# Performance work log

Measured on AMD Instinct MI355X. Metric: run time of the kernel, lower is better.

## Reference

```python
import jax, jax.numpy as jnp
import numpy as np

N = 32768          # total nodes
B = 64             # graphs
NPG = N // B       # nodes per graph (equal-sized graphs)
E = 524288         # edges (before self-loops)
D_IN, HID, HEADS, D_OUT = 128, 64, 4, 128
DH = HID * HEADS   # 256
NEG_SLOPE = 0.2
EPS = 1e-5

def _leaky(x):
    return jnp.where(x >= 0, x, NEG_SLOPE * x)

def gat_conv(x, src, dst, W, a_src, a_dst, b, concat):
    """PyG-style GATConv (self-loops already included in src/dst)."""
    H, C = a_src.shape
    h = (x @ W).reshape(N, H, C)                       # [N,H,C]
    es = jnp.einsum('nhc,hc->nh', h, a_src)            # score from source feats
    ed = jnp.einsum('nhc,hc->nh', h, a_dst)            # score from target feats
    e = _leaky(es[src] + ed[dst])                      # [E',H]
    m = jax.ops.segment_max(e, dst, num_segments=N)    # stable softmax per dst
    p = jnp.exp(e - m[dst])
    s = jax.ops.segment_sum(p, dst, num_segments=N)
    alpha = p / s[dst]                                 # [E',H]
    out = jax.ops.segment_sum(h[src] * alpha[..., None], dst, num_segments=N)
    out = out.reshape(N, H * C) if concat else out.mean(axis=1)
    return out + b

def mha(x, Wi, bi, Wo, bo, heads):
    """torch.nn.MultiheadAttention (batch_first, no mask, eval)."""
    Bb, T, D = x.shape
    qkv = x @ Wi.T + bi                                # [B,T,3D]
    q, k, v = jnp.split(qkv, 3, axis=-1)
    hd = D // heads
    def sp(t):
        return t.reshape(Bb, T, heads, hd).transpose(0, 2, 1, 3)  # [B,h,T,hd]
    q, k, v = sp(q), sp(k), sp(v)
    scores = jnp.einsum('bhqd,bhkd->bhqk', q, k) / jnp.sqrt(jnp.float32(hd))
    attn = jax.nn.softmax(scores, axis=-1)
    o = jnp.einsum('bhqk,bhkd->bhqd', attn, v)
    o = o.transpose(0, 2, 1, 3).reshape(Bb, T, D)
    return o @ Wo.T + bo

def layer_norm(x, g, b):
    mu = x.mean(-1, keepdims=True)
    var = x.var(-1, keepdims=True)
    return (x - mu) / jnp.sqrt(var + EPS) * g + b

def setup_inputs() -> dict:
    key = jax.random.key(0)
    ks = jax.random.split(key, 20)
    s = 0.1
    inp = {
        'x': jax.random.normal(ks[0], (N, D_IN), jnp.float32),
        'edge_index': jax.random.randint(ks[1], (2, E), 0, N, jnp.int64),
        'batch': (jnp.arange(N, dtype=jnp.int64) // NPG),
        # gat1: D_IN -> HEADS*HID (concat)
        'W1': jax.random.normal(ks[2], (D_IN, HEADS * HID), jnp.float32) * s,
        'aS1': jax.random.normal(ks[3], (HEADS, HID), jnp.float32) * s,
        'aD1': jax.random.normal(ks[4], (HEADS, HID), jnp.float32) * s,
        'b1': jnp.zeros((HEADS * HID,), jnp.float32),
        # gat2: DH -> HEADS*HID (concat)
        'W2': jax.random.normal(ks[5], (DH, HEADS * HID), jnp.float32) * s,
        'aS2': jax.random.normal(ks[6], (HEADS, HID), jnp.float32) * s,
        'aD2': jax.random.normal(ks[7], (HEADS, HID), jnp.float32) * s,
        'b2': jnp.zeros((HEADS * HID,), jnp.float32),
        # gat3: DH -> D_OUT, heads=1, concat=False (mean)
        'W3': jax.random.normal(ks[8], (DH, D_OUT), jnp.float32) * s,
        'aS3': jax.random.normal(ks[9], (1, D_OUT), jnp.float32) * s,
        'aD3': jax.random.normal(ks[10], (1, D_OUT), jnp.float32) * s,
        'b3': jnp.zeros((D_OUT,), jnp.float32),
        # MultiheadAttention
        'Wi': jax.random.normal(ks[11], (3 * DH, DH), jnp.float32) * s,
        'bi': jnp.zeros((3 * DH,), jnp.float32),
        'Wo': jax.random.normal(ks[12], (DH, DH), jnp.float32) * s,
        'bo': jnp.zeros((DH,), jnp.float32),
        # LayerNorm
        'gamma': jnp.ones((DH,), jnp.float32),
        'beta': jnp.zeros((DH,), jnp.float32),
    }
    return inp

def reference(x, edge_index, batch, W1, aS1, aD1, b1, W2, aS2, aD2, b2,
              W3, aS3, aD3, b3, Wi, bi, Wo, bo, gamma, beta):
    # add self-loops (PyG GATConv default)
    loops = jnp.arange(N, dtype=edge_index.dtype)
    src = jnp.concatenate([edge_index[0], loops])
    dst = jnp.concatenate([edge_index[1], loops])

    x1 = jax.nn.elu(gat_conv(x, src, dst, W1, aS1, aD1, b1, concat=True))
    x2 = jax.nn.elu(gat_conv(x1, src, dst, W2, aS2, aD2, b2, concat=True))

    # ragged-to-dense batching: batch = arange(N)//NPG (equal-sized, sorted),
    # so the torch python loop reduces to a reshape with no padding.
    x2b = x2.reshape(B, NPG, DH)
    attended = mha(x2b, Wi, bi, Wo, bo, HEADS).reshape(N, DH)

    x2a = layer_norm(attended + x2, gamma, beta)
    x3 = gat_conv(x2a, src, dst, W3, aS3, aD3, b3, concat=False)
    return x3
```

## Files before the change

kernel.cpp:

```cpp
#include <hip/hip_runtime.h>

typedef _Float16 half_t;
typedef _Float16 half8  __attribute__((ext_vector_type(8)));
typedef _Float16 half4v __attribute__((ext_vector_type(4)));
typedef _Float16 half2v __attribute__((ext_vector_type(2)));
typedef float    f32x4  __attribute__((ext_vector_type(4)));
typedef float    f32x2  __attribute__((ext_vector_type(2)));

constexpr int N_NODES = 32768;
constexpr int NPG_    = 512;

#define MFMA16(a, b, c) __builtin_amdgcn_mfma_f32_16x16x32_f16((a), (b), (c), 0, 0, 0)

#if defined(__has_builtin)
#  if __has_builtin(__builtin_amdgcn_cvt_pk_f16_fp8)
#    define HAVE_PK_F16_FP8 1
#  else
#    define HAVE_PK_F16_FP8 0
#  endif
#else
#  define HAVE_PK_F16_FP8 0
#endif

__device__ __forceinline__ void gload_lds16(const half_t* g, half_t* l) {
  __builtin_amdgcn_global_load_lds(
      (const __attribute__((address_space(1))) void*)g,
      (__attribute__((address_space(3))) void*)l, 16, 0, 0);
}

__device__ __forceinline__ void fp8x4_fma(int wrd, half2v p, half2v* acc) {
#if HAVE_PK_F16_FP8
  half2v lo = __builtin_amdgcn_cvt_pk_f16_fp8((short)(wrd & 0xffff));
  half2v hi = __builtin_amdgcn_cvt_pk_f16_fp8((short)(((unsigned)wrd) >> 16));
#else
  f32x2 flo = __builtin_amdgcn_cvt_pk_f32_fp8(wrd, false);
  f32x2 fhi = __builtin_amdgcn_cvt_pk_f32_fp8(wrd, true);
  half2v lo = {(half_t)flo.x, (half_t)flo.y};
  half2v hi = {(half_t)fhi.x, (half_t)fhi.y};
#endif
  acc[0] += p * lo;
  acc[1] += p * hi;
}

__global__ __launch_bounds__(256) void k_scan1(const int* __restrict__ deg,
                                               int* __restrict__ partial,
                                               int* __restrict__ blockSums) {
  __shared__ int sd[256];
  int t = threadIdx.x;
  int i = blockIdx.x * 256 + t;
  int v = deg[i] + 1;
  sd[t] = v;
  __syncthreads();
  int acc = v;
  for (int off = 1; off < 256; off <<= 1) {
    int add = (t >= off) ? sd[t - off] : 0;
    __syncthreads();
    acc += add;
    sd[t] = acc;
    __syncthreads();
  }
  partial[i] = acc - v;
  if (t == 255) blockSums[blockIdx.x] = acc;
}

__global__ __launch_bounds__(128) void k_scan2(const int* __restrict__ blockSums,
                                               int* __restrict__ blockOff,
                                               int* __restrict__ rowptr) {
  __shared__ int sd[128];
  int t = threadIdx.x;
  int v = blockSums[t];
  sd[t] = v;
  __syncthreads();
  for (int off = 1; off < 128; off <<= 1) {
    int add = (t >= off) ? sd[t - off] : 0;
    __syncthreads();
    sd[t] += add;
    __syncthreads();
  }
  blockOff[t] = sd[t] - v;
  if (t == 127) rowptr[N_NODES] = sd[t];
}

__global__ __launch_bounds__(256) void k_scan3(const int* __restrict__ partial,
                                               const int* __restrict__ blockOff,
                                               int* __restrict__ rowptr,
                                               int* __restrict__ fill,
                                               int* __restrict__ col) {
  int i = blockIdx.x * 256 + threadIdx.x;
  int rp = partial[i] + blockOff[blockIdx.x];
  rowptr[i] = rp;
  fill[i] = 1;
  col[rp] = i;
}

__global__ void k_scatter(const int* __restrict__ src, const int* __restrict__ dst,
                          const int* __restrict__ rowptr, int* __restrict__ fill,
                          int* __restrict__ col, int E) {
  int i = blockIdx.x * 256 + threadIdx.x;
  if (i < E) {
    int d = dst[i];
    int pos = rowptr[d] + atomicAdd(&fill[d], 1);
    col[pos] = src[i];
  }
}

__global__ void k_convert(
    const float* __restrict__ x,  half_t* __restrict__ x_h,
    const float* __restrict__ W1, half_t* __restrict__ W1t,
    const float* __restrict__ W2, half_t* __restrict__ W2t,
    const float* __restrict__ W3, half_t* __restrict__ W3t,
    const float* __restrict__ Wi, half_t* __restrict__ Wi_h,
    const float* __restrict__ Wo, half_t* __restrict__ Wo_h,
    const int* __restrict__ dst, int* __restrict__ deg, int E)
{
  int bid = blockIdx.x, t = threadIdx.x;
  if (bid < 4096) {
    int i = bid * 256 + t;
    float4 v = *(const float4*)(x + (size_t)i * 4);
    half4v h = {(half_t)v.x, (half_t)v.y, (half_t)v.z, (half_t)v.w};
    *(half4v*)(x_h + (size_t)i * 4) = h;
  } else if (bid < 4224) {
    int i = (bid - 4096) * 256 + t;
    int o = i >> 7, k = i & 127;
    W1t[i] = (half_t)W1[k * 256 + o];
  } else if (bid < 4480) {
    int i = (bid - 4224) * 256 + t;
    int o = i >> 8, k = i & 255;
    W2t[i] = (half_t)W2[k * 256 + o];
  } else if (bid < 4608) {
    int i = (bid - 4480) * 256 + t;
    int o = i >> 8, k = i & 255;
    W3t[i] = (half_t)W3[k * 128 + o];
  } else if (bid < 4800) {
    int i = (bid - 4608) * 256 + t;
    float4 v = *(const float4*)(Wi + (size_t)i * 4);
    half4v h = {(half_t)v.x, (half_t)v.y, (half_t)v.z, (half_t)v.w};
    *(half4v*)(Wi_h + (size_t)i * 4) = h;
  } else if (bid < 4864) {
    int i = (bid - 4800) * 256 + t;
    float4 v = *(const float4*)(Wo + (size_t)i * 4);
    half4v h = {(half_t)v.x, (half_t)v.y, (half_t)v.z, (half_t)v.w};
    *(half4v*)(Wo_h + (size_t)i * 4) = h;
  } else {
    int i = (bid - 4864) * 256 + t;
    if (i < E) atomicAdd(&deg[dst[i]], 1);
  }
}

__device__ __forceinline__ void gemm_wide_body(
    int bx, int by,
    const half_t* __restrict__ A, const half_t* __restrict__ Bt,
    const float* __restrict__ bias, int bias_per_row,
    half_t* __restrict__ outh, int Nc, int K,
    half_t* As, half_t* Bs)
{
  int w = threadIdx.x >> 6, lane = threadIdx.x & 63;
  int r = lane & 15, q = lane >> 4;
  int m0 = by * 128, n0 = bx * 64;
  int mh = (w & 1) * 64, nh = (w >> 1) * 32;
  f32x4 acc[4][2];
  #pragma unroll
  for (int i = 0; i < 4; i++)
    #pragma unroll
    for (int j = 0; j < 2; j++) acc[i][j] = f32x4{0.f, 0.f, 0.f, 0.f};

  int srow = lane >> 3, sc = lane & 7;

  for (int k0 = 0; k0 < K; k0 += 64) {
    __syncthreads();
    #pragma unroll
    for (int i = 0; i < 4; i++) {
      int R0 = w * 32 + i * 8;
      int row = R0 + srow;
      int cg = sc ^ (row & 7);
      gload_lds16(A + (size_t)(m0 + row) * K + k0 + cg * 8, &As[R0 * 64]);
    }
    #pragma unroll
    for (int i = 0; i < 2; i++) {
      int R0 = w * 16 + i * 8;
      int row = R0 + srow;
      int cg = sc ^ (row & 7);
      gload_lds16(Bt + (size_t)(n0 + row) * K + k0 + cg * 8, &Bs[R0 * 64]);
    }
    __syncthreads();
    #pragma unroll
    for (int kk = 0; kk < 2; kk++) {
      half8 af[4], bf[2];
      #pragma unroll
      for (int t = 0; t < 4; t++) {
        int rr = mh + t * 16 + r;
        af[t] = *(const half8*)&As[rr * 64 + (((kk * 4 + q) ^ (rr & 7)) << 3)];
      }
      #pragma unroll
      for (int t = 0; t < 2; t++) {
        int rr = nh + t * 16 + r;
        bf[t] = *(const half8*)&Bs[rr * 64 + (((kk * 4 + q) ^ (rr & 7)) << 3)];
      }
      #pragma unroll
      for (int ti = 0; ti < 4; ti++)
        #pragma unroll
        for (int tj = 0; tj < 2; tj++)
          acc[ti][tj] = MFMA16(af[ti], bf[tj], acc[ti][tj]);
    }
  }

  #pragma unroll
  for (int tj = 0; tj < 2; tj++) {
    int colc = n0 + nh + tj * 16 + r;
    float bc = bias_per_row ? 0.f : bias[colc];
    #pragma unroll
    for (int ti = 0; ti < 4; ti++) {
      #pragma unroll
      for (int i = 0; i < 4; i++) {
        int row = m0 + mh + ti * 16 + q * 4 + i;
        float bv = bias_per_row ? bias[row] : bc;
        outh[(size_t)row * Nc + colc] = (half_t)(acc[ti][tj][i] + bv);
      }
    }
  }
}

__global__ __launch_bounds__(256) void k_gemm_qkv2(
    const half_t* __restrict__ x2, const half_t* __restrict__ Wi_h,
    const float* __restrict__ bi,
    half_t* __restrict__ qk, half_t* __restrict__ vt)
{
  __shared__ __align__(16) half_t As[128 * 64];
  __shared__ __align__(16) half_t Bs[64 * 64];
  int id = blockIdx.x;
  if (id < 2048) {
    gemm_wide_body(id & 7, id >> 3, x2, Wi_h, bi, 0, qk, 512, 256, As, Bs);
  } else {
    int id2 = id - 2048;
    gemm_wide_body(id2 & 511, id2 >> 9, Wi_h + 512 * 256, x2, bi + 512, 1,
                   vt, 32768, 256, As, Bs);
  }
}

template<int NC, int H, bool FP8O>
__global__ __launch_bounds__(256) void k_gemm_gat(
    const half_t* __restrict__ A, const half_t* __restrict__ Bt,
    half_t* __restrict__ outh, unsigned char* __restrict__ out8, int K,
    const float* __restrict__ aS, const float* __restrict__ aD,
    float* __restrict__ es, float* __restrict__ ed)
{
  __shared__ __align__(16) half_t As[128 * 64];
  __shared__ __align__(16) half_t Bs[64 * 64];
  __shared__ float sRed[2][4][64];
  int w = threadIdx.x >> 6, lane = threadIdx.x & 63;
  int cc = lane & 15, qq = lane >> 4;
  int m0 = blockIdx.y * 128, n0 = blockIdx.x * 64;
  int mh = (w & 1) * 64, nh = (w >> 1) * 32;
  f32x4 acc[4][2];
  #pragma unroll
  for (int i = 0; i < 4; i++)
    #pragma unroll
    for (int j = 0; j < 2; j++) acc[i][j] = f32x4{0.f, 0.f, 0.f, 0.f};

  int srow = lane >> 3, sc = lane & 7;

  for (int k0 = 0; k0 < K; k0 += 64) {
    __syncthreads();
    #pragma unroll
    for (int i = 0; i < 4; i++) {
      int R0 = w * 32 + i * 8;
      int row = R0 + srow;
      int cg = sc ^ (row & 7);
      gload_lds16(A + (size_t)(m0 + row) * K + k0 + cg * 8, &As[R0 * 64]);
    }
    #pragma unroll
    for (int i = 0; i < 2; i++) {
      int R0 = w * 16 + i * 8;
      int row = R0 + srow;
      int cg = sc ^ (row & 7);
      gload_lds16(Bt + (size_t)(n0 + row) * K + k0 + cg * 8, &Bs[R0 * 64]);
    }
    __syncthreads();
    #pragma unroll
    for (int kk = 0; kk < 2; kk++) {
      half8 af[4], bf[2];
      #pragma unroll
      for (int t = 0; t < 4; t++) {
        int rr = mh + t * 16 + cc;
        af[t] = *(const half8*)&As[rr * 64 + (((kk * 4 + qq) ^ (rr & 7)) << 3)];
      }
      #pragma unroll
      for (int t = 0; t < 2; t++) {
        int rr = nh + t * 16 + cc;
        bf[t] = *(const half8*)&Bs[rr * 64 + (((kk * 4 + qq) ^ (rr & 7)) << 3)];
      }
      #pragma unroll
      for (int ti = 0; ti < 4; ti++)
        #pragma unroll
        for (int tj = 0; tj < 2; tj++)
          acc[ti][tj] = MFMA16(af[ti], bf[tj], acc[ti][tj]);
    }
  }

  float aSv[2], aDv[2];
  #pragma unroll
  for (int tj = 0; tj < 2; tj++) {
    int colg = n0 + nh + tj * 16 + cc;
    aSv[tj] = aS[colg];
    aDv[tj] = aD[colg];
  }
  #pragma unroll
  for (int ti = 0; ti < 4; ti++) {
    #pragma unroll
    for (int i = 0; i < 4; i++) {
      int rloc = mh + ti * 16 + qq * 4 + i;
      float ps = 0.f, pd = 0.f;
      #pragma unroll
      for (int tj = 0; tj < 2; tj++) {
        int colg = n0 + nh + tj * 16 + cc;
        float v = acc[ti][tj][i];
        if (FP8O) {
          int pk = __builtin_amdgcn_cvt_pk_fp8_f32(v, v, 0, false);
          out8[(size_t)(m0 + rloc) * NC + colg] = (unsigned char)pk;
        } else {
          outh[(size_t)(m0 + rloc) * NC + colg] = (half_t)v;
        }
        ps += v * aSv[tj];
        pd += v * aDv[tj];
      }
      #pragma unroll
      for (int off = 1; off < 16; off <<= 1) {
        ps += __shfl_xor(ps, off);
        pd += __shfl_xor(pd, off);
      }
      if (cc == 0) {
        sRed[0][w][ti * 16 + qq * 4 + i] = ps;
        sRed[1][w][ti * 16 + qq * 4 + i] = pd;
      }
    }
  }
  __syncthreads();
  if (threadIdx.x < 128) {
    int row = threadIdx.x;
    int wlo = row >> 6, ri = row & 63;
    float ps = sRed[0][wlo][ri] + sRed[0][wlo + 2][ri];
    float pd = sRed[1][wlo][ri] + sRed[1][wlo + 2][ri];
    if (H == 4) {
      int head = n0 >> 6;
      es[(size_t)(m0 + row) * 4 + head] = ps;
      ed[(size_t)(m0 + row) * 4 + head] = pd;
    } else {
      atomicAdd(&es[m0 + row], ps);
      atomicAdd(&ed[m0 + row], pd);
    }
  }
}

__global__ __launch_bounds__(256) void k_gemm_ln(
    const half_t* __restrict__ A, const half_t* __restrict__ Bt,
    const float* __restrict__ bias, const half_t* __restrict__ res,
    const float* __restrict__ gamma, const float* __restrict__ beta,
    half_t* __restrict__ outh, float* __restrict__ es0, float* __restrict__ ed0)
{
  __shared__ __align__(16) half_t As[64 * 64];
  __shared__ __align__(16) half_t Bs[256 * 64];
  __shared__ float sSum[4][64], sSq[4][64];
  __shared__ float sMR[64][2];
  int w = threadIdx.x >> 6, lane = threadIdx.x & 63;
  int r = lane & 15, q = lane >> 4;
  int m0 = blockIdx.x * 64;
  int nh = w * 64;

  if (threadIdx.x < 64) es0[m0 + threadIdx.x] = 0.f;
  else if (threadIdx.x < 128) ed0[m0 + threadIdx.x - 64] = 0.f;

  f32x4 acc[4][4];
  #pragma unroll
  for (int i = 0; i < 4; i++)
    #pragma unroll
    for (int j = 0; j < 4; j++) acc[i][j] = f32x4{0.f, 0.f, 0.f, 0.f};

  int srow = lane >> 3, sc = lane & 7;

  for (int k0 = 0; k0 < 256; k0 += 64) {
    __syncthreads();
    #pragma unroll
    for (int i = 0; i < 2; i++) {
      int R0 = w * 16 + i * 8;
      int row = R0 + srow;
      int cg = sc ^ (row & 7);
      gload_lds16(A + (size_t)(m0 + row) * 256 + k0 + cg * 8, &As[R0 * 64]);
    }
    #pragma unroll
    for (int i = 0; i < 8; i++) {
      int R0 = w * 64 + i * 8;
      int row = R0 + srow;
      int cg = sc ^ (row & 7);
      gload_lds16(Bt + (size_t)row * 256 + k0 + cg * 8, &Bs[R0 * 64]);
    }
    __syncthreads();
    #pragma unroll
    for (int kk = 0; kk < 2; kk++) {
      half8 af[4], bf[4];
      #pragma unroll
      for (int t = 0; t < 4; t++) {
        int rr = t * 16 + r;
        af[t] = *(const half8*)&As[rr * 64 + (((kk * 4 + q) ^ (rr & 7)) << 3)];
      }
      #pragma unroll
      for (int t = 0; t < 4; t++) {
        int rr = nh + t * 16 + r;
        bf[t] = *(const half8*)&Bs[rr * 64 + (((kk * 4 + q) ^ (rr & 7)) << 3)];
      }
      #pragma unroll
      for (int ti = 0; ti < 4; ti++)
        #pragma unroll
        for (int tj = 0; tj < 4; tj++)
          acc[ti][tj] = MFMA16(af[ti], bf[tj], acc[ti][tj]);
    }
  }

  float gv[4], bv[4];
  #pragma unroll
  for (int tj = 0; tj < 4; tj++) {
    int col = nh + tj * 16 + r;
    gv[tj] = gamma[col];
    bv[tj] = beta[col];
  }
  #pragma unroll
  for (int ti = 0; ti < 4; ti++) {
    #pragma unroll
    for (int i = 0; i < 4; i++) {
      int row = ti * 16 + q * 4 + i;
      float s = 0.f, ss = 0.f;
      #pragma unroll
      for (int tj = 0; tj < 4; tj++) {
        int col = nh + tj * 16 + r;
        float v = acc[ti][tj][i] + bias[col]
                + (float)res[(size_t)(m0 + row) * 256 + col];
        acc[ti][tj][i] = v;
        s += v;
        ss += v * v;
      }
      #pragma unroll
      for (int off = 1; off < 16; off <<= 1) {
        s  += __shfl_xor(s, off);
        ss += __shfl_xor(ss, off);
      }
      if (r == 0) { sSum[w][row] = s; sSq[w][row] = ss; }
    }
  }
  __syncthreads();
  if (threadIdx.x < 64) {
    int row = threadIdx.x;
    float s  = sSum[0][row] + sSum[1][row] + sSum[2][row] + sSum[3][row];
    float ss = sSq[0][row] + sSq[1][row] + sSq[2][row] + sSq[3][row];
    float mean = s * (1.f / 256.f);
    float var  = ss * (1.f / 256.f) - mean * mean;
    sMR[row][0] = mean;
    sMR[row][1] = rsqrtf(var + 1e-5f);
  }
  __syncthreads();
  #pragma unroll
  for (int ti = 0; ti < 4; ti++) {
    #pragma unroll
    for (int i = 0; i < 4; i++) {
      int row = ti * 16 + q * 4 + i;
      float mean = sMR[row][0], rstd = sMR[row][1];
      #pragma unroll
      for (int tj = 0; tj < 4; tj++) {
        int col = nh + tj * 16 + r;
        outh[(size_t)(m0 + row) * 256 + col] =
            (half_t)((acc[ti][tj][i] - mean) * rstd * gv[tj] + bv[tj]);
      }
    }
  }
}

__global__ __launch_bounds__(256) void k_agg_f16(
    const half_t* __restrict__ h, const float* __restrict__ es,
    const float* __restrict__ ed, const float* __restrict__ bias,
    const int* __restrict__ rowptr, const int* __restrict__ col,
    half_t* __restrict__ outh)
{
  int lane = threadIdx.x & 63;
  int g = lane >> 4, li = lane & 15;
  int n = blockIdx.x * 4 + (threadIdx.x >> 6);
  int cbase = li * 16;
  int hl = li >> 2;
  float edn = ed[(size_t)n * 4 + hl];
  int j0 = rowptr[n], j1 = rowptr[n + 1];
  const half_t* hb = h + cbase;

  float sum0 = 0.f, sum1 = 0.f;
  half8 acc0[2], acc1[2];
  #pragma unroll
  for (int i = 0; i < 2; i++) {
    acc0[i] = half8{0, 0, 0, 0, 0, 0, 0, 0};
    acc1[i] = half8{0, 0, 0, 0, 0, 0, 0, 0};
  }
  for (int j = j0 + g; j < j1; j += 8) {
    int jb = j + 4;
    int s0 = col[j];
    int s1 = col[(jb < j1) ? jb : j];
    float e0 = es[(size_t)s0 * 4 + hl] + edn;
    e0 = fmaxf(e0, 0.2f * e0);
    float e1 = es[(size_t)s1 * 4 + hl] + edn;
    e1 = fmaxf(e1, 0.2f * e1);
    e1 = (jb < j1) ? e1 : -1e30f;
    const half_t* hp0 = hb + (size_t)s0 * 256;
    const half_t* hp1 = hb + (size_t)s1 * 256;
    float p0 = exp2f(e0 * 1.44269504f - 8.65617025f);
    float p1 = exp2f(e1 * 1.44269504f - 8.65617025f);
    sum0 += p0; sum1 += p1;
    half_t q0 = (half_t)p0, q1 = (half_t)p1;
    half8 pv0 = {q0, q0, q0, q0, q0, q0, q0, q0};
    half8 pv1 = {q1, q1, q1, q1, q1, q1, q1, q1};
    #pragma unroll
    for (int i = 0; i < 2; i++) {
      half8 v0 = *(const half8*)(hp0 + i * 8);
      half8 v1 = *(const half8*)(hp1 + i * 8);
      acc0[i] += pv0 * v0;
      acc1[i] += pv1 * v1;
    }
  }
  float sum = sum0 + sum1;
  sum += __shfl_xor(sum, 16);
  sum += __shfl_xor(sum, 32);
  float av[16];
  #pragma unroll
  for (int i = 0; i < 16; i++) {
    av[i] = (float)acc0[i >> 3][i & 7] + (float)acc1[i >> 3][i & 7];
    av[i] += __shfl_xor(av[i], 16);
    av[i] += __shfl_xor(av[i], 32);
  }
  float inv = 1.f / sum;
  if (g == 0) {
    size_t obase = (size_t)n * 256 + cbase;
    #pragma unroll
    for (int p8 = 0; p8 < 2; p8++) {
      half8 hv;
      #pragma unroll
      for (int i = 0; i < 8; i++) {
        float t = av[p8 * 8 + i] * inv + bias[cbase + p8 * 8 + i];
        t = (t > 0.f) ? t : __expf(t) - 1.f;
        hv[i] = (half_t)t;
      }
      *(half8*)(outh + obase + p8 * 8) = hv;
    }
  }
}

__global__ __launch_bounds__(256) void k_agg_fp8(
    const unsigned char* __restrict__ hq, const float* __restrict__ es,
    const float* __restrict__ ed, const float* __restrict__ bias,
    const int* __restrict__ rowptr, const int* __restrict__ col,
    half_t* __restrict__ outh)
{
  int lane = threadIdx.x & 63;
  int g = lane >> 4, li = lane & 15;
  int n = blockIdx.x * 4 + (threadIdx.x >> 6);
  int cbase = li * 16;
  int hl = li >> 2;
  float edn = ed[(size_t)n * 4 + hl];
  int j0 = rowptr[n], j1 = rowptr[n + 1];
  const unsigned char* hb = hq + cbase;

  float sum0 = 0.f, sum1 = 0.f;
  half2v a0[8], a1[8];
  #pragma unroll
  for (int i = 0; i < 8; i++) { a0[i] = half2v{0, 0}; a1[i] = half2v{0, 0}; }

  for (int j = j0 + g; j < j1; j += 8) {
    int jb = j + 4;
    int s0 = col[j];
    int s1 = col[(jb < j1) ? jb : j];
    float e0 = es[(size_t)s0 * 4 + hl] + edn;
    e0 = fmaxf(e0, 0.2f * e0);
    float e1 = es[(size_t)s1 * 4 + hl] + edn;
    e1 = fmaxf(e1, 0.2f * e1);
    e1 = (jb < j1) ? e1 : -1e30f;
    int4 d0 = *(const int4*)(hb + (size_t)s0 * 256);
    int4 d1 = *(const int4*)(hb + (size_t)s1 * 256);
    float p0 = exp2f(e0 * 1.44269504f - 8.65617025f);
    float p1 = exp2f(e1 * 1.44269504f - 8.65617025f);
    sum0 += p0; sum1 += p1;
    half_t q0 = (half_t)p0, q1 = (half_t)p1;
    half2v pv0 = {q0, q0}, pv1 = {q1, q1};
    fp8x4_fma(d0.x, pv0, &a0[0]); fp8x4_fma(d0.y, pv0, &a0[2]);
    fp8x4_fma(d0.z, pv0, &a0[4]); fp8x4_fma(d0.w, pv0, &a0[6]);
    fp8x4_fma(d1.x, pv1, &a1[0]); fp8x4_fma(d1.y, pv1, &a1[2]);
    fp8x4_fma(d1.z, pv1, &a1[4]); fp8x4_fma(d1.w, pv1, &a1[6]);
  }

  float sum = sum0 + sum1;
  sum += __shfl_xor(sum, 16);
  sum += __shfl_xor(sum, 32);
  float av[16];
  #pragma unroll
  for (int i = 0; i < 16; i++) {
    av[i] = (float)a0[i >> 1][i & 1] + (float)a1[i >> 1][i & 1];
    av[i] += __shfl_xor(av[i], 16);
    av[i] += __shfl_xor(av[i], 32);
  }
  float inv = 1.f / sum;
  if (g == 0) {
    size_t obase = (size_t)n * 256 + cbase;
    #pragma unroll
    for (int p8 = 0; p8 < 2; p8++) {
      half8 hv;
      #pragma unroll
      for (int i = 0; i < 8; i++) {
        float t = av[p8 * 8 + i] * inv + bias[cbase + p8 * 8 + i];
        t = (t > 0.f) ? t : __expf(t) - 1.f;
        hv[i] = (half_t)t;
      }
      *(half8*)(outh + obase + p8 * 8) = hv;
    }
  }
}

__global__ __launch_bounds__(256) void k_agg3(
    const half_t* __restrict__ h, const float* __restrict__ es,
    const float* __restrict__ ed, const float* __restrict__ bias,
    const int* __restrict__ rowptr, const int* __restrict__ col,
    float* __restrict__ outf)
{
  constexpr int VPT = 8;
  int lane = threadIdx.x & 63;
  int g = lane >> 4, li = lane & 15;
  int n = blockIdx.x * 4 + (threadIdx.x >> 6);
  int cbase = li * VPT;
  float edn = ed[n];
  int j0 = rowptr[n], j1 = rowptr[n + 1];
  const half_t* hb = h + cbase;

  float sum0 = 0.f, sum1 = 0.f;
  float acc0[VPT], acc1[VPT];
  #pragma unroll
  for (int i = 0; i < VPT; i++) { acc0[i] = 0.f; acc1[i] = 0.f; }
  for (int j = j0 + g; j < j1; j += 8) {
    int jb = j + 4;
    int s0 = col[j];
    int s1 = col[(jb < j1) ? jb : j];
    float e0 = es[s0] + edn;
    e0 = fmaxf(e0, 0.2f * e0);
    float e1 = es[s1] + edn;
    e1 = fmaxf(e1, 0.2f * e1);
    e1 = (jb < j1) ? e1 : -1e30f;
    const half_t* hp0 = hb + (size_t)s0 * 128;
    const half_t* hp1 = hb + (size_t)s1 * 128;
    float p0 = __expf(e0), p1 = __expf(e1);
    sum0 += p0; sum1 += p1;
    half8 v0 = *(const half8*)hp0;
    half8 v1 = *(const half8*)hp1;
    #pragma unroll
    for (int i = 0; i < 8; i++) {
      acc0[i] += p0 * (float)v0[i];
      acc1[i] += p1 * (float)v1[i];
    }
  }
  float sum = sum0 + sum1;
  sum += __shfl_xor(sum, 16);
  sum += __shfl_xor(sum, 32);
  float av[VPT];
  #pragma unroll
  for (int i = 0; i < VPT; i++) {
    av[i] = acc0[i] + acc1[i];
    av[i] += __shfl_xor(av[i], 16);
    av[i] += __shfl_xor(av[i], 32);
  }
  float inv = 1.f / sum;
  if (g == 0) {
    size_t obase = (size_t)n * 128 + cbase;
    #pragma unroll
    for (int p4 = 0; p4 < 2; p4++) {
      float4 fv = {av[p4 * 4] * inv + bias[cbase + p4 * 4],
                   av[p4 * 4 + 1] * inv + bias[cbase + p4 * 4 + 1],
                   av[p4 * 4 + 2] * inv + bias[cbase + p4 * 4 + 2],
                   av[p4 * 4 + 3] * inv + bias[cbase + p4 * 4 + 3]};
      *(float4*)(outf + obase + p4 * 4) = fv;
    }
  }
}

__global__ __launch_bounds__(256) void k_attn(
    const half_t* __restrict__ qk, const half_t* __restrict__ vt,
    half_t* __restrict__ o)
{
  __shared__ __align__(16) half_t Kt[64 * 64];
  __shared__ __align__(16) half_t Vt[64 * 64];
  __shared__ __align__(16) half_t Pb[4][16][72];

  int pair = blockIdx.x;
  int b = pair >> 2, hh = pair & 3;
  int q0 = blockIdx.y * 64;
  int w = threadIdx.x >> 6, lane = threadIdx.x & 63;
  int cc = lane & 15, qq = lane >> 4;

  const half_t* Qp = qk + ((size_t)(b * NPG_ + q0 + w * 16 + cc) * 512 + hh * 64);
  half8 qa0 = *(const half8*)(Qp + qq * 8);
  half8 qa1 = *(const half8*)(Qp + 32 + qq * 8);

  f32x4 oacc[4];
  #pragma unroll
  for (int t = 0; t < 4; t++) oacc[t] = f32x4{0.f, 0.f, 0.f, 0.f};
  float rs = 0.f;

  const half_t* kb = qk + ((size_t)(b * NPG_) * 512 + 256 + hh * 64);
  const half_t* vb = vt + ((size_t)(hh * 64) * 32768 + b * NPG_);

  int krow = lane >> 3, ksl = lane & 7;

  for (int kt = 0; kt < 8; kt++) {
    __syncthreads();
    #pragma unroll
    for (int i = 0; i < 2; i++) {
      int R = w * 16 + i * 8;
      int kr = R + krow;
      gload_lds16(kb + (size_t)(kt * 64 + kr) * 512 + ((ksl ^ (kr & 7)) * 8),
                  &Kt[R * 64]);
      gload_lds16(vb + (size_t)kr * 32768 + kt * 64 + ((ksl ^ (kr & 7)) * 8),
                  &Vt[R * 64]);
    }
    __syncthreads();

    #pragma unroll
    for (int mt = 0; mt < 4; mt++) {
      int key = mt * 16 + cc;
      half8 k0 = *(const half8*)&Kt[key * 64 + ((qq ^ (key & 7)) << 3)];
      half8 k1 = *(const half8*)&Kt[key * 64 + (((qq + 4) ^ (key & 7)) << 3)];
      f32x4 s = f32x4{0.f, 0.f, 0.f, 0.f};
      s = MFMA16(k0, qa0, s);
      s = MFMA16(k1, qa1, s);
      half4v ph;
      #pragma unroll
      for (int i = 0; i < 4; i++) {
        float p = exp2f(s[i] * 0.180336886f - 11.54156033f);
        rs += p;
        ph[i] = (half_t)p;
      }
      *(half4v*)&Pb[w][cc][mt * 16 + qq * 4] = ph;
    }

    #pragma unroll
    for (int kc = 0; kc < 2; kc++) {
      half8 a = *(const half8*)&Pb[w][cc][kc * 32 + qq * 8];
      #pragma unroll
      for (int nt = 0; nt < 4; nt++) {
        int d = nt * 16 + cc;
        half8 bb = *(const half8*)&Vt[d * 64 + (((kc * 4 + qq) ^ (d & 7)) << 3)];
        oacc[nt] = MFMA16(a, bb, oacc[nt]);
      }
    }
  }

  rs += __shfl_xor(rs, 16);
  rs += __shfl_xor(rs, 32);
  #pragma unroll
  for (int i = 0; i < 4; i++) {
    float rsv = __shfl(rs, qq * 4 + i);
    float inv = 1.f / rsv;
    int node = b * NPG_ + q0 + w * 16 + qq * 4 + i;
    #pragma unroll
    for (int nt = 0; nt < 4; nt++)
      o[(size_t)node * 256 + hh * 64 + nt * 16 + cc] = (half_t)(oacc[nt][i] * inv);
  }
}

extern "C" void kernel_launch(void* const* d_in, const int* in_sizes, int n_in,
                              void* d_out, int out_size, void* d_ws, size_t ws_size,
                              hipStream_t stream)
{
  const float* x    = (const float*)d_in[0];
  const int*   ei   = (const int*)d_in[1];
  const float* W1   = (const float*)d_in[3];
  const float* aS1  = (const float*)d_in[4];
  const float* aD1  = (const float*)d_in[5];
  const float* b1   = (const float*)d_in[6];
  const float* W2   = (const float*)d_in[7];
  const float* aS2  = (const float*)d_in[8];
  const float* aD2  = (const float*)d_in[9];
  const float* b2   = (const float*)d_in[10];
  const float* W3   = (const float*)d_in[11];
  const float* aS3  = (const float*)d_in[12];
  const float* aD3  = (const float*)d_in[13];
  const float* b3   = (const float*)d_in[14];
  const float* Wi   = (const float*)d_in[15];
  const float* bi   = (const float*)d_in[16];
  const float* Wo   = (const float*)d_in[17];
  const float* bo   = (const float*)d_in[18];
  const float* gam  = (const float*)d_in[19];
  const float* bet  = (const float*)d_in[20];
  float* out = (float*)d_out;
  const int N = N_NODES;
  int E = in_sizes[1] / 2;

  char* ws = (char*)d_ws;
  size_t off = 0;
  auto alloc = [&](size_t bytes) -> void* {
    void* p = ws + off;
    off = (off + bytes + 255) & ~(size_t)255;
    return p;
  };
  half_t* x_h    = (half_t*)alloc((size_t)N * 128 * 2);
  half_t* h_h    = (half_t*)alloc((size_t)N * 256 * 2);
  unsigned char* hq = (unsigned char*)alloc((size_t)N * 256);
  half_t* x1_h   = (half_t*)alloc((size_t)N * 256 * 2);
  half_t* x2_h   = (half_t*)alloc((size_t)N * 256 * 2);
  half_t* qk_h   = (half_t*)alloc((size_t)N * 512 * 2);
  half_t* vt_h   = (half_t*)alloc((size_t)256 * N * 2);
  half_t* o_h    = (half_t*)alloc((size_t)N * 256 * 2);
  half_t* x2a_h  = (half_t*)alloc((size_t)N * 256 * 2);
  half_t* W1t    = (half_t*)alloc(256 * 128 * 2);
  half_t* W2t    = (half_t*)alloc(256 * 256 * 2);
  half_t* W3t    = (half_t*)alloc(128 * 256 * 2);
  half_t* Wi_h   = (half_t*)alloc(768 * 256 * 2);
  half_t* Wo_h   = (half_t*)alloc(256 * 256 * 2);
  float*  es     = (float*) alloc((size_t)N * 4 * 4);
  float*  ed     = (float*) alloc((size_t)N * 4 * 4);
  int*    deg    = (int*)   alloc((size_t)N * 4);
  int*    fill   = (int*)   alloc((size_t)N * 4);
  int*    rowptr = (int*)   alloc(((size_t)N + 1) * 4);
  int*    col    = (int*)   alloc((size_t)(N + E) * 4);
  int*    part   = (int*)   alloc((size_t)N * 4);
  int*    bsum   = (int*)   alloc(128 * 4);
  int*    boff   = (int*)   alloc(128 * 4);

  const int* srcE = ei;
  const int* dstE = ei + E;

  hipMemsetAsync(deg, 0, (size_t)N * 4, stream);
  int convGrid = 4864 + (E + 255) / 256;
  k_convert<<<convGrid, 256, 0, stream>>>(x, x_h, W1, W1t, W2, W2t, W3, W3t,
                                          Wi, Wi_h, Wo, Wo_h, dstE, deg, E);
  k_scan1<<<128, 256, 0, stream>>>(deg, part, bsum);
  k_scan2<<<1, 128, 0, stream>>>(bsum, boff, rowptr);
  k_scan3<<<128, 256, 0, stream>>>(part, boff, rowptr, fill, col);
  k_scatter<<<(E + 255) / 256, 256, 0, stream>>>(srcE, dstE, rowptr, fill, col, E);

  k_gemm_gat<256, 4, false><<<dim3(4, N / 128), 256, 0, stream>>>(
      x_h, W1t, h_h, nullptr, 128, aS1, aD1, es, ed);
  k_agg_f16<<<N / 4, 256, 0, stream>>>(h_h, es, ed, b1, rowptr, col, x1_h);

  k_gemm_gat<256, 4, true><<<dim3(4, N / 128), 256, 0, stream>>>(
      x1_h, W2t, nullptr, hq, 256, aS2, aD2, es, ed);
  k_agg_fp8<<<N / 4, 256, 0, stream>>>(hq, es, ed, b2, rowptr, col, x2_h);

  k_gemm_qkv2<<<3072, 256, 0, stream>>>(x2_h, Wi_h, bi, qk_h, vt_h);
  k_attn<<<dim3(256, 8), 256, 0, stream>>>(qk_h, vt_h, o_h);

  k_gemm_ln<<<N / 64, 256, 0, stream>>>(o_h, Wo_h, bo, x2_h, gam, bet, x2a_h, es, ed);

  k_gemm_gat<128, 1, false><<<dim3(2, N / 128), 256, 0, stream>>>(
      x2a_h, W3t, h_h, nullptr, 256, aS3, aD3, es, ed);
  k_agg3<<<N / 4, 256, 0, stream>>>(h_h, es, ed, b3, rowptr, col, out);
}
```

Before: 388.8 us.

## Merge scan stages and fuse edge scatter into first GAT GEMM launch

Folds the single-block block-sum scan into the final scan kernel by having every block redundantly scan the 128 block sums. Moves the CSR edge scatter into extra blocks appended to the first GAT GEMM grid so that it runs alongside the GEMM instead of as a separate launch. This removes two kernel launches and their serialization gaps. In exchange, each block repeats a small scan, and the GEMM kernel gains extra parameters and a branch.

Result: no change. 387.9 us (-0.2%).

```diff
diff --git a/kernel.cpp b/kernel.cpp
--- a/kernel.cpp
+++ b/kernel.cpp
@@ -63,45 +63,27 @@
   if (t == 255) blockSums[blockIdx.x] = acc;
 }
 
-__global__ __launch_bounds__(128) void k_scan2(const int* __restrict__ blockSums,
-                                               int* __restrict__ blockOff,
-                                               int* __restrict__ rowptr) {
+__global__ __launch_bounds__(256) void k_scan23(
+    const int* __restrict__ partial, const int* __restrict__ blockSums,
+    int* __restrict__ rowptr, int* __restrict__ fill, int* __restrict__ col)
+{
   __shared__ int sd[128];
   int t = threadIdx.x;
-  int v = blockSums[t];
-  sd[t] = v;
+  if (t < 128) sd[t] = blockSums[t];
   __syncthreads();
   for (int off = 1; off < 128; off <<= 1) {
-    int add = (t >= off) ? sd[t - off] : 0;
-    __syncthreads();
-    sd[t] += add;
-    __syncthreads();
-  }
-  blockOff[t] = sd[t] - v;
-  if (t == 127) rowptr[N_NODES] = sd[t];
-}
-
-__global__ __launch_bounds__(256) void k_scan3(const int* __restrict__ partial,
-                                               const int* __restrict__ blockOff,
-                                               int* __restrict__ rowptr,
-                                               int* __restrict__ fill,
-                                               int* __restrict__ col) {
-  int i = blockIdx.x * 256 + threadIdx.x;
-  int rp = partial[i] + blockOff[blockIdx.x];
+    int add = (t < 128 && t >= off) ? sd[t - off] : 0;
+    __syncthreads();
+    if (t < 128) sd[t] += add;
+    __syncthreads();
+  }
+  int bo = (blockIdx.x == 0) ? 0 : sd[blockIdx.x - 1];
+  int i = blockIdx.x * 256 + t;
+  int rp = partial[i] + bo;
   rowptr[i] = rp;
   fill[i] = 1;
   col[rp] = i;
-}
-
-__global__ void k_scatter(const int* __restrict__ src, const int* __restrict__ dst,
-                          const int* __restrict__ rowptr, int* __restrict__ fill,
-                          int* __restrict__ col, int E) {
-  int i = blockIdx.x * 256 + threadIdx.x;
-  if (i < E) {
-    int d = dst[i];
-    int pos = rowptr[d] + atomicAdd(&fill[d], 1);
-    col[pos] = src[i];
-  }
+  if (blockIdx.x == 127 && t == 255) rowptr[N_NODES] = sd[127];
 }
 
 __global__ void k_convert(
@@ -237,16 +219,31 @@
   }
 }
 
-template<int NC, int H, bool FP8O>
+template<int NC, int H, bool FP8O, bool FUSE_SCAT>
 __global__ __launch_bounds__(256) void k_gemm_gat(
     const half_t* __restrict__ A, const half_t* __restrict__ Bt,
     half_t* __restrict__ outh, unsigned char* __restrict__ out8, int K,
     const float* __restrict__ aS, const float* __restrict__ aD,
-    float* __restrict__ es, float* __restrict__ ed)
+    float* __restrict__ es, float* __restrict__ ed,
+    const int* __restrict__ srcE, const int* __restrict__ dstE,
+    const int* __restrict__ rowptr, int* __restrict__ fill,
+    int* __restrict__ col, int E)
 {
   __shared__ __align__(16) half_t As[128 * 64];
   __shared__ __align__(16) half_t Bs[64 * 64];
   __shared__ float sRed[2][4][64];
+
+  if (FUSE_SCAT && (int)blockIdx.y >= N_NODES / 128) {
+    int i = (((int)blockIdx.y - N_NODES / 128) * 4 + (int)blockIdx.x) * 256
+            + (int)threadIdx.x;
+    if (i < E) {
+      int d = dstE[i];
+      int pos = rowptr[d] + atomicAdd(&fill[d], 1);
+      col[pos] = srcE[i];
+    }
+    return;
+  }
+
   int w = threadIdx.x >> 6, lane = threadIdx.x & 63;
   int cc = lane & 15, qq = lane >> 4;
   int m0 = blockIdx.y * 128, n0 = blockIdx.x * 64;
@@ -820,7 +817,6 @@
   int*    col    = (int*)   alloc((size_t)(N + E) * 4);
   int*    part   = (int*)   alloc((size_t)N * 4);
   int*    bsum   = (int*)   alloc(128 * 4);
-  int*    boff   = (int*)   alloc(128 * 4);
 
   const int* srcE = ei;
   const int* dstE = ei + E;
@@ -830,16 +826,17 @@
   k_convert<<<convGrid, 256, 0, stream>>>(x, x_h, W1, W1t, W2, W2t, W3, W3t,
                                           Wi, Wi_h, Wo, Wo_h, dstE, deg, E);
   k_scan1<<<128, 256, 0, stream>>>(deg, part, bsum);
-  k_scan2<<<1, 128, 0, stream>>>(bsum, boff, rowptr);
-  k_scan3<<<128, 256, 0, stream>>>(part, boff, rowptr, fill, col);
-  k_scatter<<<(E + 255) / 256, 256, 0, stream>>>(srcE, dstE, rowptr, fill, col, E);
-
-  k_gemm_gat<256, 4, false><<<dim3(4, N / 128), 256, 0, stream>>>(
-      x_h, W1t, h_h, nullptr, 128, aS1, aD1, es, ed);
+  k_scan23<<<128, 256, 0, stream>>>(part, bsum, rowptr, fill, col);
+
+  int eyr = (E + 1023) / 1024;
+  k_gemm_gat<256, 4, false, true><<<dim3(4, N / 128 + eyr), 256, 0, stream>>>(
+      x_h, W1t, h_h, nullptr, 128, aS1, aD1, es, ed,
+      srcE, dstE, rowptr, fill, col, E);
   k_agg_f16<<<N / 4, 256, 0, stream>>>(h_h, es, ed, b1, rowptr, col, x1_h);
 
-  k_gemm_gat<256, 4, true><<<dim3(4, N / 128), 256, 0, stream>>>(
-      x1_h, W2t, nullptr, hq, 256, aS2, aD2, es, ed);
+  k_gemm_gat<256, 4, true, false><<<dim3(4, N / 128), 256, 0, stream>>>(
+      x1_h, W2t, nullptr, hq, 256, aS2, aD2, es, ed,
+      nullptr, nullptr, nullptr, nullptr, nullptr, 0);
   k_agg_fp8<<<N / 4, 256, 0, stream>>>(hq, es, ed, b2, rowptr, col, x2_h);
 
   k_gemm_qkv2<<<3072, 256, 0, stream>>>(x2_h, Wi_h, bi, qk_h, vt_h);
@@ -847,7 +844,8 @@
 
   k_gemm_ln<<<N / 64, 256, 0, stream>>>(o_h, Wo_h, bo, x2_h, gam, bet, x2a_h, es, ed);
 
-  k_gemm_gat<128, 1, false><<<dim3(2, N / 128), 256, 0, stream>>>(
-      x2a_h, W3t, h_h, nullptr, 256, aS3, aD3, es, ed);
+  k_gemm_gat<128, 1, false, false><<<dim3(2, N / 128), 256, 0, stream>>>(
+      x2a_h, W3t, h_h, nullptr, 256, aS3, aD3, es, ed,
+      nullptr, nullptr, nullptr, nullptr, nullptr, 0);
   k_agg3<<<N / 4, 256, 0, stream>>>(h_h, es, ed, b3, rowptr, col, out);
 }
```
